# Kernel tuning notes

Measured on AMD Instinct MI355X. Metric: run time of the kernel, lower is better.

## Reference

```python
import jax, jax.numpy as jnp
import numpy as np
from jax.scipy.special import logsumexp

EPS = 1e-6
SINKHORN_ITERS = 8
TEMPERATURE = 1.0


def sinkhorn(logits):
    # log(clamp(t, min=eps)) / temperature, then alternating row/col log-normalization
    t = jnp.log(jnp.clip(logits, EPS)) / TEMPERATURE
    for _ in range(SINKHORN_ITERS):
        t = t - logsumexp(t, axis=-2, keepdims=True)  # over tokens n
        t = t - logsumexp(t, axis=-1, keepdims=True)  # over experts e
    return jnp.exp(t)


def setup_inputs() -> dict:
    key = jax.random.key(0)
    k1, k2, k3 = jax.random.split(key, 3)
    b, n, d, e, h = 4, 4096, 1024, 8, 1
    x = jax.random.normal(k1, (b, n, d), dtype=jnp.float32)
    gate_w = jax.random.normal(k2, (h, d, e), dtype=jnp.float32)  # to_gate_weight
    experts = jax.random.normal(k3, (e, d, d), dtype=jnp.float32) * 0.02  # expert weight tensor [e, i, o]
    return {"x": x, "gate_w": gate_w, "experts": experts}


def reference(x, gate_w, experts):
    b, n, d = x.shape
    h, _, e = gate_w.shape
    m = n // e  # tokens_per_expert

    xh = x[:, None]  # b 1 n d  (single-headed path)

    # gate logits: b h n e
    gate_logits = jnp.einsum('bhnd,hde->bhne', xh, gate_w)

    # competitive sinkhorn gates (eval mode, no gumbel noise)
    gates = sinkhorn(gate_logits)

    # topk over token dim (dim=-2) with k = tokens_per_expert
    g = jnp.swapaxes(gates, -1, -2)          # b h e n
    gv, idx = jax.lax.top_k(g, m)            # b h e m
    gate_values = jnp.swapaxes(gv, -1, -2)   # b h m e
    routed_indices = jnp.swapaxes(idx, -1, -2)  # b h m e

    # eval + competitive -> hard gates
    hard_gates = (gate_values > 0.5).astype(x.dtype)  # b h m e

    # gather routed tokens: routed[b,h,m,e,d] = x[b,h,idx[b,h,m,e],d]
    bi = jnp.arange(b)[:, None, None, None]
    hi = jnp.arange(h)[None, :, None, None]
    routed = xh[bi, hi, routed_indices]  # b h m e d

    # per-expert GEMM, vectorized over experts: experts [e,i,o] -> [e,h,i,o]
    experts4 = experts[:, None, :, :]
    out = jnp.einsum('bhmei,ehio->bhmeo', routed, experts4)  # b h m e o

    # weight by gates
    out = out * hard_gates[..., None]

    # scatter back (set semantics, as in einx set_at)
    y = jnp.zeros_like(xh).at[bi, hi, routed_indices].set(out)  # b h n d
    return y[:, 0]  # b n d
```

## Files before the change

### kernel.cpp

```cpp
#include <hip/hip_runtime.h>
#include <hip/hip_bf16.h>
#include <stdint.h>

#define BB 4
#define NN 4096
#define DD 1024
#define EE 8
#define MM 512
#define BN (BB*NN)

#define FRONT_GATE 512
#define FRONT_CONV 2048
#define SKBLK 4

typedef __bf16 bf16x8 __attribute__((ext_vector_type(8)));
typedef float  floatx4 __attribute__((ext_vector_type(4)));

typedef const __attribute__((address_space(1))) void* gptr_t;
typedef __attribute__((address_space(3))) void* lptr_t;

__device__ __forceinline__ unsigned short f2bf(float f) {
    union { float f; unsigned u; } v; v.f = f;
    unsigned r = v.u + 0x7fffu + ((v.u >> 16) & 1u);
    return (unsigned short)(r >> 16);
}

__device__ __forceinline__ float gate_reduce8(const float acc[8], int lane) {
    float k1[4];
#pragma unroll
    for (int e = 0; e < 4; e++) {
        float a = acc[e]     + __shfl_xor(acc[e],     1, 64);
        float b = acc[e + 4] + __shfl_xor(acc[e + 4], 1, 64);
        k1[e] = (lane & 1) ? b : a;
    }
    float k2[2];
#pragma unroll
    for (int e = 0; e < 2; e++) {
        float a = k1[e]     + __shfl_xor(k1[e],     2, 64);
        float b = k1[e + 2] + __shfl_xor(k1[e + 2], 2, 64);
        k2[e] = (lane & 2) ? b : a;
    }
    float a = k2[0] + __shfl_xor(k2[0], 4, 64);
    float b = k2[1] + __shfl_xor(k2[1], 4, 64);
    float v = (lane & 4) ? b : a;
    v += __shfl_xor(v, 8, 64);
    v += __shfl_xor(v, 16, 64);
    v += __shfl_xor(v, 32, 64);
    return v;
}

#define OFF_GATES   0u
#define OFF_COUNTS  655360u
#define OFF_LISTS   655616u
#define OFF_KEYS    753920u
#define OFF_XBF     1802496u
#define OFF_EXPT    35356928u
#define WS_NEEDED   52134144u

__global__ __launch_bounds__(256, 2) void gate_kernel(const float* __restrict__ x,
                                                      const float* __restrict__ gw,
                                                      float* __restrict__ tmat,
                                                      unsigned short* __restrict__ xbf,
                                                      int* __restrict__ counts) {
    int bid = blockIdx.x;
    int tid = threadIdx.x;
    if (bid >= FRONT_GATE) {
        if (tid < 32) counts[tid] = 0;
        return;
    }
    int wave = tid >> 6, lane = tid & 63;
    float4 g0[4][4], g1[4][4];
#pragma unroll
    for (int j = 0; j < 4; j++)
#pragma unroll
        for (int r = 0; r < 4; r++) {
            const float4* p = (const float4*)(gw + (size_t)(j * 256 + lane * 4 + r) * 8);
            g0[j][r] = p[0];
            g1[j][r] = p[1];
        }
    int tok0 = (bid * 4 + wave) * 8;
    int exp_id = ((lane & 1) << 2) | (lane & 2) | ((lane & 4) >> 2);

    float4 xa[4], xc[4], na[4], nc[4];
    {
        const float4* xr = (const float4*)(x + (size_t)tok0 * DD);
#pragma unroll
        for (int j = 0; j < 4; j++) xa[j] = xr[j * 64 + lane];
#pragma unroll
        for (int j = 0; j < 4; j++) xc[j] = xr[256 + j * 64 + lane];
    }
#pragma unroll
    for (int tt = 0; tt < 8; tt += 2) {
        int tokA = tok0 + tt, tokB = tokA + 1;
        if (tt < 6) {
            const float4* xrn = (const float4*)(x + (size_t)(tokA + 2) * DD);
#pragma unroll
            for (int j = 0; j < 4; j++) na[j] = xrn[j * 64 + lane];
#pragma unroll
            for (int j = 0; j < 4; j++) nc[j] = xrn[256 + j * 64 + lane];
        }
        if (xbf) {
#pragma unroll
            for (int j = 0; j < 4; j++) {
                ushort4 o;
                o.x = f2bf(xa[j].x); o.y = f2bf(xa[j].y); o.z = f2bf(xa[j].z); o.w = f2bf(xa[j].w);
                ((ushort4*)(xbf + (size_t)tokA * DD))[j * 64 + lane] = o;
            }
#pragma unroll
            for (int j = 0; j < 4; j++) {
                ushort4 o;
                o.x = f2bf(xc[j].x); o.y = f2bf(xc[j].y); o.z = f2bf(xc[j].z); o.w = f2bf(xc[j].w);
                ((ushort4*)(xbf + (size_t)tokB * DD))[j * 64 + lane] = o;
            }
        }
        float accA[8] = {0.f, 0.f, 0.f, 0.f, 0.f, 0.f, 0.f, 0.f};
        float accB[8] = {0.f, 0.f, 0.f, 0.f, 0.f, 0.f, 0.f, 0.f};
#pragma unroll
        for (int j = 0; j < 4; j++) {
            accA[0] += xa[j].x * g0[j][0].x + xa[j].y * g0[j][1].x + xa[j].z * g0[j][2].x + xa[j].w * g0[j][3].x;
            accA[1] += xa[j].x * g0[j][0].y + xa[j].y * g0[j][1].y + xa[j].z * g0[j][2].y + xa[j].w * g0[j][3].y;
            accA[2] += xa[j].x * g0[j][0].z + xa[j].y * g0[j][1].z + xa[j].z * g0[j][2].z + xa[j].w * g0[j][3].z;
            accA[3] += xa[j].x * g0[j][0].w + xa[j].y * g0[j][1].w + xa[j].z * g0[j][2].w + xa[j].w * g0[j][3].w;
            accA[4] += xa[j].x * g1[j][0].x + xa[j].y * g1[j][1].x + xa[j].z * g1[j][2].x + xa[j].w * g1[j][3].x;
            accA[5] += xa[j].x * g1[j][0].y + xa[j].y * g1[j][1].y + xa[j].z * g1[j][2].y + xa[j].w * g1[j][3].y;
            accA[6] += xa[j].x * g1[j][0].z + xa[j].y * g1[j][1].z + xa[j].z * g1[j][2].z + xa[j].w * g1[j][3].z;
            accA[7] += xa[j].x * g1[j][0].w + xa[j].y * g1[j][1].w + xa[j].z * g1[j][2].w + xa[j].w * g1[j][3].w;
            accB[0] += xc[j].x * g0[j][0].x + xc[j].y * g0[j][1].x + xc[j].z * g0[j][2].x + xc[j].w * g0[j][3].x;
            accB[1] += xc[j].x * g0[j][0].y + xc[j].y * g0[j][1].y + xc[j].z * g0[j][2].y + xc[j].w * g0[j][3].y;
            accB[2] += xc[j].x * g0[j][0].z + xc[j].y * g0[j][1].z + xc[j].z * g0[j][2].z + xc[j].w * g0[j][3].z;
            accB[3] += xc[j].x * g0[j][0].w + xc[j].y * g0[j][1].w + xc[j].z * g0[j][2].w + xc[j].w * g0[j][3].w;
            accB[4] += xc[j].x * g1[j][0].x + xc[j].y * g1[j][1].x + xc[j].z * g1[j][2].x + xc[j].w * g1[j][3].x;
            accB[5] += xc[j].x * g1[j][0].y + xc[j].y * g1[j][1].y + xc[j].z * g1[j][2].y + xc[j].w * g1[j][3].y;
            accB[6] += xc[j].x * g1[j][0].z + xc[j].y * g1[j][1].z + xc[j].z * g1[j][2].z + xc[j].w * g1[j][3].z;
            accB[7] += xc[j].x * g1[j][0].w + xc[j].y * g1[j][1].w + xc[j].z * g1[j][2].w + xc[j].w * g1[j][3].w;
        }
        float vA = gate_reduce8(accA, lane);
        float vB = gate_reduce8(accB, lane);
        if (lane < 8) {
            tmat[(size_t)tokA * EE + exp_id] = logf(fmaxf(vA, 1e-6f));
            tmat[(size_t)tokB * EE + exp_id] = logf(fmaxf(vB, 1e-6f));
        }
        if (tt < 6) {
#pragma unroll
            for (int j = 0; j < 4; j++) { xa[j] = na[j]; xc[j] = nc[j]; }
        }
    }
}

__global__ __launch_bounds__(512) void sinkhorn_conv(const float* __restrict__ tmat,
                                                     unsigned long long* __restrict__ keys,
                                                     int* __restrict__ rank,
                                                     const float* __restrict__ E,
                                                     unsigned short* __restrict__ expt) {
    __shared__ float tile[64][65];
    __shared__ float red[8][8];
    __shared__ float bcm[8];
    int g = blockIdx.x;
    int tid = threadIdx.x;

    if (g >= SKBLK) {
        if (!expt) return;
        int cb = g - SKBLK;
        int e = cb >> 8, t = cb & 255;
        int k0 = (t >> 4) * 64, c0 = (t & 15) * 64;
        int r = tid >> 3, c8 = (tid & 7) * 8;
        const float* src = E + ((size_t)e * DD + k0 + r) * DD + c0 + c8;
        float4 v0 = *(const float4*)src;
        float4 v1 = *(const float4*)(src + 4);
        tile[r][c8 + 0] = v0.x; tile[r][c8 + 1] = v0.y; tile[r][c8 + 2] = v0.z; tile[r][c8 + 3] = v0.w;
        tile[r][c8 + 4] = v1.x; tile[r][c8 + 5] = v1.y; tile[r][c8 + 6] = v1.z; tile[r][c8 + 7] = v1.w;
        __syncthreads();
        int cc = tid >> 3, kk8 = (tid & 7) * 8;
        ushort4 o0, o1;
        o0.x = f2bf(tile[kk8 + 0][cc]); o0.y = f2bf(tile[kk8 + 1][cc]);
        o0.z = f2bf(tile[kk8 + 2][cc]); o0.w = f2bf(tile[kk8 + 3][cc]);
        o1.x = f2bf(tile[kk8 + 4][cc]); o1.y = f2bf(tile[kk8 + 5][cc]);
        o1.z = f2bf(tile[kk8 + 6][cc]); o1.w = f2bf(tile[kk8 + 7][cc]);
        unsigned short* dst = expt + ((size_t)e * DD + c0 + cc) * DD + k0 + kk8;
        *(ushort4*)dst = o0;
        *(ushort4*)(dst + 4) = o1;
        return;
    }

    int b = g;
    int wave = tid >> 6, lane = tid & 63;
    const float* tb = tmat + (size_t)b * NN * EE;
    float tv[8][8];
#pragma unroll
    for (int k = 0; k < 8; k++) {
        const float4* p = (const float4*)(tb + (size_t)(k * 512 + tid) * EE);
        float4 v0 = p[0], v1 = p[1];
        tv[k][0] = v0.x; tv[k][1] = v0.y; tv[k][2] = v0.z; tv[k][3] = v0.w;
        tv[k][4] = v1.x; tv[k][5] = v1.y; tv[k][6] = v1.z; tv[k][7] = v1.w;
    }

    for (int it = 0; it < 8; it++) {
        float ls[8];
#pragma unroll
        for (int e = 0; e < 8; e++) {
            float s = 0.f;
#pragma unroll
            for (int k = 0; k < 8; k++) s += expf(tv[k][e]);
            ls[e] = s;
        }
        float r8 = gate_reduce8(ls, lane);
        if (lane < 8) {
            int eid = ((lane & 1) << 2) | (lane & 2) | ((lane & 4) >> 2);
            red[wave][eid] = r8;
        }
        __syncthreads();
        if (tid < 8) {
            float s = 0.f;
#pragma unroll
            for (int w = 0; w < 8; w++) s += red[w][tid];
            bcm[tid] = logf(s);
        }
        __syncthreads();
        float bl[8];
#pragma unroll
        for (int e = 0; e < 8; e++) bl[e] = bcm[e];
#pragma unroll
        for (int k = 0; k < 8; k++) {
            float s = 0.f;
#pragma unroll
            for (int e = 0; e < 8; e++) { tv[k][e] -= bl[e]; s += expf(tv[k][e]); }
            float lse = logf(s);
#pragma unroll
            for (int e = 0; e < 8; e++) tv[k][e] -= lse;
        }
    }
#pragma unroll
    for (int k = 0; k < 8; k++) {
        int row = k * 512 + tid;
#pragma unroll
        for (int e = 0; e < 8; e++) {
            unsigned fb = __float_as_uint(expf(tv[k][e]));
            keys[(size_t)(b * EE + e) * NN + row] =
                ((unsigned long long)fb << 32) | (unsigned)(~row);
        }
    }
    {
        int4* rz = (int4*)(rank + (size_t)b * EE * NN);
        int4 z4 = make_int4(0, 0, 0, 0);
#pragma unroll
        for (int q = 0; q < 16; q++) rz[q * 512 + tid] = z4;
    }
}

__global__ __launch_bounds__(256) void rank_count_kernel(const unsigned long long* __restrict__ keys,
                                                         int* __restrict__ rank) {
    int be = blockIdx.y;
    int tid = threadIdx.x;
    int t = blockIdx.x * 256 + tid;
    const unsigned long long* kcol = keys + (size_t)be * NN;
    unsigned long long my = kcol[t];
    const unsigned long long* ks = kcol + (size_t)blockIdx.z * (NN / 4);

    int c0 = 0, c1 = 0, c2 = 0, c3 = 0;
    for (int j = 0; j < NN / 4; j += 16) {
#pragma unroll
        for (int i = 0; i < 16; i += 4) {
            c0 += (int)(ks[j + i + 0] > my);
            c1 += (int)(ks[j + i + 1] > my);
            c2 += (int)(ks[j + i + 2] > my);
            c3 += (int)(ks[j + i + 3] > my);
        }
    }
    atomicAdd(&rank[(size_t)be * NN + t], (c0 + c1) + (c2 + c3));
}

__global__ __launch_bounds__(256) void build_zero_kernel(const unsigned long long* __restrict__ keys,
                                                         const int* __restrict__ rank,
                                                         int* __restrict__ counts,
                                                         int* __restrict__ lists,
                                                         float* __restrict__ y) {
    __shared__ int act_s[64];
    int base = blockIdx.x * 64;
    int tid = threadIdx.x;
    if (tid < 64) {
        int i = base + tid;
        int b = i >> 12, tok = i & 4095;
        int wmax = -1;
#pragma unroll
        for (int e = 0; e < EE; e++) {
            int r = rank[(size_t)(b * 8 + e) * NN + tok];
            if (r < MM) {
                int w = r * 8 + e;
                wmax = wmax > w ? wmax : w;
            }
        }
        int active = 0;
        if (wmax >= 0) {
            int ew = wmax & 7;
            unsigned hi = (unsigned)(keys[(size_t)(b * 8 + ew) * NN + tok] >> 32);
            if (__uint_as_float(hi) > 0.5f) {
                int p = atomicAdd(&counts[b * 8 + ew], 1);
                lists[(b * 8 + ew) * MM + p] = tok;
                active = 1;
            }
        }
        act_s[tid] = active;
    }
    __syncthreads();
    float4 z = make_float4(0.f, 0.f, 0.f, 0.f);
    for (int r = 0; r < 64; r++) {
        if (!act_s[r])
            ((float4*)(y + (size_t)(base + r) * DD))[tid] = z;
    }
}

__global__ __launch_bounds__(256) void expert_gemm_mfma(const unsigned short* __restrict__ xbf,
                                                        const unsigned short* __restrict__ expt,
                                                        const int* __restrict__ counts,
                                                        const int* __restrict__ lists,
                                                        float* __restrict__ y) {
    int be = blockIdx.z;
    int b = be >> 3, e = be & 7;
    int cnt = counts[be];
    int row0 = blockIdx.y * 64;
    if (row0 >= cnt) return;
    int col0 = blockIdx.x * 128;

    __shared__ unsigned short As[64 * 32];
    __shared__ unsigned short Bs[128 * 32];
    __shared__ int toks[64];

    int tid = threadIdx.x;
    int wave = tid >> 6, lane = tid & 63;
    int m16 = lane & 15, quad = lane >> 4;
    int wave_m = wave >> 1, wave_n = wave & 1;

    if (tid < 64) {
        int r = row0 + tid;
        toks[tid] = lists[be * MM + (r < cnt ? r : cnt - 1)];
    }

    int r0 = tid >> 2;
    int ch = tid & 3;

    const unsigned short* xb = xbf + (size_t)b * NN * DD;
    const unsigned short* Eb = expt + (size_t)e * DD * DD;

    floatx4 acc[2][4];
#pragma unroll
    for (int i = 0; i < 2; i++)
#pragma unroll
        for (int j = 0; j < 4; j++) acc[i][j] = (floatx4)0.f;

    for (int k0 = 0; k0 < DD; k0 += 32) {
        __syncthreads();
        {
            const unsigned short* gA  = xb + (size_t)toks[r0] * DD + k0 + ch * 8;
            const unsigned short* gB0 = Eb + (size_t)(col0 + r0) * DD + k0 + ch * 8;
            const unsigned short* gB1 = Eb + (size_t)(col0 + 64 + r0) * DD + k0 + ch * 8;
            __builtin_amdgcn_global_load_lds((gptr_t)gA,  (lptr_t)(As + (size_t)tid * 8), 16, 0, 0);
            __builtin_amdgcn_global_load_lds((gptr_t)gB0, (lptr_t)(Bs + (size_t)tid * 8), 16, 0, 0);
            __builtin_amdgcn_global_load_lds((gptr_t)gB1, (lptr_t)(Bs + 64 * 32 + (size_t)tid * 8), 16, 0, 0);
        }
        __syncthreads();
        bf16x8 af[2], bfr[4];
#pragma unroll
        for (int i = 0; i < 2; i++)
            af[i] = *(const bf16x8*)&As[(wave_m * 32 + i * 16 + m16) * 32 + quad * 8];
#pragma unroll
        for (int j = 0; j < 4; j++)
            bfr[j] = *(const bf16x8*)&Bs[(wave_n * 64 + j * 16 + m16) * 32 + quad * 8];
#pragma unroll
        for (int i = 0; i < 2; i++)
#pragma unroll
            for (int j = 0; j < 4; j++)
                acc[i][j] = __builtin_amdgcn_mfma_f32_16x16x32_bf16(af[i], bfr[j], acc[i][j], 0, 0, 0);
    }

#pragma unroll
    for (int i = 0; i < 2; i++) {
#pragma unroll
        for (int r = 0; r < 4; r++) {
            int lr = wave_m * 32 + i * 16 + quad * 4 + r;
            if (row0 + lr < cnt) {
                int tok = toks[lr];
                float* yr = y + ((size_t)b * NN + tok) * DD + col0 + wave_n * 64 + m16;
#pragma unroll
                for (int j = 0; j < 4; j++) yr[j * 16] = acc[i][j][r];
            }
        }
    }
}

__global__ __launch_bounds__(256) void expert_gemm_kernel(const float* __restrict__ x,
                                                          const float* __restrict__ experts,
                                                          const int* __restrict__ counts,
                                                          const int* __restrict__ lists,
                                                          float* __restrict__ y) {
    int be = blockIdx.z;
    int b = be >> 3, e = be & 7;
    int cnt = counts[be];
    int row0 = blockIdx.y * 64;
    if (row0 >= cnt) return;
    int col0 = blockIdx.x * 64;
    __shared__ float As2[16][68];
    __shared__ float Bs2[16][68];
    __shared__ int toks[64];
    int tid = threadIdx.x;
    if (tid < 64) {
        int r = row0 + tid;
        toks[tid] = (r < cnt) ? lists[be * MM + r] : -1;
    }
    __syncthreads();
    int tx = tid & 15, ty = tid >> 4;
    int ar = tid >> 2;
    int ak = (tid & 3) * 4;
    int bk = tid >> 4;
    int bc4 = (tid & 15) * 4;
    int atok = toks[ar];
    const float* xb = x + (size_t)b * NN * DD;
    const float* Eb = experts + (size_t)e * DD * DD + col0;
    float acc[4][4] = {};
    for (int k0 = 0; k0 < DD; k0 += 16) {
        float4 av;
        if (atok >= 0) av = *(const float4*)(xb + (size_t)atok * DD + k0 + ak);
        else av = make_float4(0.f, 0.f, 0.f, 0.f);
        float4 bv = *(const float4*)(Eb + (size_t)(k0 + bk) * DD + bc4);
        __syncthreads();
        As2[ak + 0][ar] = av.x; As2[ak + 1][ar] = av.y; As2[ak + 2][ar] = av.z; As2[ak + 3][ar] = av.w;
        *(float4*)&Bs2[bk][bc4] = bv;
        __syncthreads();
#pragma unroll
        for (int kk = 0; kk < 16; kk++) {
            float4 a = *(const float4*)&As2[kk][ty * 4];
            float4 bb = *(const float4*)&Bs2[kk][tx * 4];
            acc[0][0] += a.x * bb.x; acc[0][1] += a.x * bb.y; acc[0][2] += a.x * bb.z; acc[0][3] += a.x * bb.w;
            acc[1][0] += a.y * bb.x; acc[1][1] += a.y * bb.y; acc[1][2] += a.y * bb.z; acc[1][3] += a.y * bb.w;
            acc[2][0] += a.z * bb.x; acc[2][1] += a.z * bb.y; acc[2][2] += a.z * bb.z; acc[2][3] += a.z * bb.w;
            acc[3][0] += a.w * bb.x; acc[3][1] += a.w * bb.y; acc[3][2] += a.w * bb.z; acc[3][3] += a.w * bb.w;
        }
    }
#pragma unroll
    for (int i = 0; i < 4; i++) {
        int rl = ty * 4 + i;
        if (row0 + rl < cnt) {
            int tok = toks[rl];
            float4 o = make_float4(acc[i][0], acc[i][1], acc[i][2], acc[i][3]);
            *(float4*)(y + ((size_t)b * NN + tok) * DD + col0 + tx * 4) = o;
        }
    }
}

extern "C" void kernel_launch(void* const* d_in, const int* in_sizes, int n_in,
                              void* d_out, int out_size, void* d_ws, size_t ws_size,
                              hipStream_t stream) {
    const float* x       = (const float*)d_in[0];
    const float* gw      = (const float*)d_in[1];
    const float* experts = (const float*)d_in[2];
    float* y = (float*)d_out;

    char* ws = (char*)d_ws;
    float*    gates    = (float*)(ws + OFF_GATES);
    int*      rank     = (int*)(ws + OFF_GATES);
    int*      counts   = (int*)(ws + OFF_COUNTS);
    int*      lists    = (int*)(ws + OFF_LISTS);
    unsigned long long* keys = (unsigned long long*)(ws + OFF_KEYS);
    bool big = ws_size >= WS_NEEDED;
    unsigned short* xbf  = big ? (unsigned short*)(ws + OFF_XBF)  : nullptr;
    unsigned short* expt = big ? (unsigned short*)(ws + OFF_EXPT) : nullptr;

    gate_kernel<<<FRONT_GATE + 1, 256, 0, stream>>>(x, gw, gates, xbf, counts);
    sinkhorn_conv<<<SKBLK + FRONT_CONV, 512, 0, stream>>>(gates, keys, rank,
                                                          experts, expt);
    rank_count_kernel<<<dim3(16, 32, 4), 256, 0, stream>>>(keys, rank);
    build_zero_kernel<<<256, 256, 0, stream>>>(keys, rank, counts, lists, y);
    if (big)
        expert_gemm_mfma<<<dim3(8, 8, BB * EE), 256, 0, stream>>>(xbf, expt, counts, lists, y);
    else
        expert_gemm_kernel<<<dim3(16, 8, BB * EE), 256, 0, stream>>>(x, experts, counts, lists, y);
}
```

Measured before the change: 299.3 us.

## Reformulate sinkhorn with column/row potentials instead of full log-matrix updates

Replaces the in-register 8x8 log-matrix that was updated every Sinkhorn iteration with a potential form. Only the column log-normalizers c[8] are carried, and each row's lse is recomputed from the original logits. Each iteration re-reads the token logits from global memory (likely cached), cutting register pressure and per-element subtract work, but it needs more expf calls per element (two passes per row). It also adds an extra __syncthreads before the rank zeroing.

```diff
diff --git a/kernel.cpp b/kernel.cpp
--- a/kernel.cpp
+++ b/kernel.cpp
@@ -47,6 +47,26 @@
     v += __shfl_xor(v, 16, 64);
     v += __shfl_xor(v, 32, 64);
     return v;
+}
+
+__device__ __forceinline__ void col_reduce(const float part[8], float c[8],
+                                           float red[8][8], float* bcm,
+                                           int wave, int lane, int tid) {
+    float r8 = gate_reduce8(part, lane);
+    if (lane < 8) {
+        int eid = ((lane & 1) << 2) | (lane & 2) | ((lane & 4) >> 2);
+        red[wave][eid] = r8;
+    }
+    __syncthreads();
+    if (tid < 8) {
+        float s = 0.f;
+#pragma unroll
+        for (int w = 0; w < 8; w++) s += red[w][tid];
+        bcm[tid] = logf(s);
+    }
+    __syncthreads();
+#pragma unroll
+    for (int e = 0; e < 8; e++) c[e] = bcm[e];
 }
 
 #define OFF_GATES   0u
@@ -185,60 +205,68 @@
     int b = g;
     int wave = tid >> 6, lane = tid & 63;
     const float* tb = tmat + (size_t)b * NN * EE;
-    float tv[8][8];
-#pragma unroll
-    for (int k = 0; k < 8; k++) {
-        const float4* p = (const float4*)(tb + (size_t)(k * 512 + tid) * EE);
-        float4 v0 = p[0], v1 = p[1];
-        tv[k][0] = v0.x; tv[k][1] = v0.y; tv[k][2] = v0.z; tv[k][3] = v0.w;
-        tv[k][4] = v1.x; tv[k][5] = v1.y; tv[k][6] = v1.z; tv[k][7] = v1.w;
-    }
-
-    for (int it = 0; it < 8; it++) {
-        float ls[8];
-#pragma unroll
-        for (int e = 0; e < 8; e++) {
-            float s = 0.f;
-#pragma unroll
-            for (int k = 0; k < 8; k++) s += expf(tv[k][e]);
-            ls[e] = s;
-        }
-        float r8 = gate_reduce8(ls, lane);
-        if (lane < 8) {
-            int eid = ((lane & 1) << 2) | (lane & 2) | ((lane & 4) >> 2);
-            red[wave][eid] = r8;
-        }
-        __syncthreads();
-        if (tid < 8) {
-            float s = 0.f;
-#pragma unroll
-            for (int w = 0; w < 8; w++) s += red[w][tid];
-            bcm[tid] = logf(s);
-        }
-        __syncthreads();
-        float bl[8];
-#pragma unroll
-        for (int e = 0; e < 8; e++) bl[e] = bcm[e];
+    float c[8];
+
+    {
+        float part[8];
+#pragma unroll
+        for (int e = 0; e < 8; e++) part[e] = 0.f;
 #pragma unroll
         for (int k = 0; k < 8; k++) {
-            float s = 0.f;
-#pragma unroll
-            for (int e = 0; e < 8; e++) { tv[k][e] -= bl[e]; s += expf(tv[k][e]); }
-            float lse = logf(s);
-#pragma unroll
-            for (int e = 0; e < 8; e++) tv[k][e] -= lse;
-        }
-    }
+            const float4* p = (const float4*)(tb + (size_t)(k * 512 + tid) * EE);
+            float4 v0 = p[0], v1 = p[1];
+            part[0] += expf(v0.x); part[1] += expf(v0.y);
+            part[2] += expf(v0.z); part[3] += expf(v0.w);
+            part[4] += expf(v1.x); part[5] += expf(v1.y);
+            part[6] += expf(v1.z); part[7] += expf(v1.w);
+        }
+        col_reduce(part, c, red, bcm, wave, lane, tid);
+    }
+
+    for (int it = 0; it < 7; it++) {
+        float part[8];
+#pragma unroll
+        for (int e = 0; e < 8; e++) part[e] = 0.f;
+#pragma unroll
+        for (int k = 0; k < 8; k++) {
+            const float4* p = (const float4*)(tb + (size_t)(k * 512 + tid) * EE);
+            float4 v0 = p[0], v1 = p[1];
+            float w0 = expf(v0.x - c[0]), w1 = expf(v0.y - c[1]);
+            float w2 = expf(v0.z - c[2]), w3 = expf(v0.w - c[3]);
+            float w4 = expf(v1.x - c[4]), w5 = expf(v1.y - c[5]);
+            float w6 = expf(v1.z - c[6]), w7 = expf(v1.w - c[7]);
+            float s = ((w0 + w1) + (w2 + w3)) + ((w4 + w5) + (w6 + w7));
+            float rk = logf(s);
+            part[0] += expf(v0.x - rk); part[1] += expf(v0.y - rk);
+            part[2] += expf(v0.z - rk); part[3] += expf(v0.w - rk);
+            part[4] += expf(v1.x - rk); part[5] += expf(v1.y - rk);
+            part[6] += expf(v1.z - rk); part[7] += expf(v1.w - rk);
+        }
+        col_reduce(part, c, red, bcm, wave, lane, tid);
+    }
+
 #pragma unroll
     for (int k = 0; k < 8; k++) {
         int row = k * 512 + tid;
-#pragma unroll
-        for (int e = 0; e < 8; e++) {
-            unsigned fb = __float_as_uint(expf(tv[k][e]));
-            keys[(size_t)(b * EE + e) * NN + row] =
-                ((unsigned long long)fb << 32) | (unsigned)(~row);
-        }
-    }
+        const float4* p = (const float4*)(tb + (size_t)row * EE);
+        float4 v0 = p[0], v1 = p[1];
+        float w0 = expf(v0.x - c[0]), w1 = expf(v0.y - c[1]);
+        float w2 = expf(v0.z - c[2]), w3 = expf(v0.w - c[3]);
+        float w4 = expf(v1.x - c[4]), w5 = expf(v1.y - c[5]);
+        float w6 = expf(v1.z - c[6]), w7 = expf(v1.w - c[7]);
+        float s = ((w0 + w1) + (w2 + w3)) + ((w4 + w5) + (w6 + w7));
+        float rk = logf(s);
+        unsigned long long rl = (unsigned)(~row);
+        keys[(size_t)(b * EE + 0) * NN + row] = ((unsigned long long)__float_as_uint(expf(v0.x - c[0] - rk)) << 32) | rl;
+        keys[(size_t)(b * EE + 1) * NN + row] = ((unsigned long long)__float_as_uint(expf(v0.y - c[1] - rk)) << 32) | rl;
+        keys[(size_t)(b * EE + 2) * NN + row] = ((unsigned long long)__float_as_uint(expf(v0.z - c[2] - rk)) << 32) | rl;
+        keys[(size_t)(b * EE + 3) * NN + row] = ((unsigned long long)__float_as_uint(expf(v0.w - c[3] - rk)) << 32) | rl;
+        keys[(size_t)(b * EE + 4) * NN + row] = ((unsigned long long)__float_as_uint(expf(v1.x - c[4] - rk)) << 32) | rl;
+        keys[(size_t)(b * EE + 5) * NN + row] = ((unsigned long long)__float_as_uint(expf(v1.y - c[5] - rk)) << 32) | rl;
+        keys[(size_t)(b * EE + 6) * NN + row] = ((unsigned long long)__float_as_uint(expf(v1.z - c[6] - rk)) << 32) | rl;
+        keys[(size_t)(b * EE + 7) * NN + row] = ((unsigned long long)__float_as_uint(expf(v1.w - c[7] - rk)) << 32) | rl;
+    }
+    __syncthreads();
     {
         int4* rz = (int4*)(rank + (size_t)b * EE * NN);
         int4 z4 = make_int4(0, 0, 0, 0);
```

Result: no change. 299.5 us (+0.1%).
